# Kernel optimization log

Hardware: AMD Instinct MI355X
Metric: run time of the kernel (lower is better)

## Reference

```python
import jax, jax.numpy as jnp
import numpy as np

N = 50000          # nodes (ogbn-products-like subgraph)
E = 800000         # directed edges (avg degree 16)
F_IN, HID, HEADS, OUT = 100, 32, 4, 47
W1 = HID * HEADS   # 128
NEG_SLOPE = 0.2
BN_EPS = 1e-5


def _gatv2(x, src, dst, w_src, w_dst, att, bias, heads, ch):
    """GATv2Conv (PyG semantics, share_weights=False, concat).
    x: [N, F]; src/dst: [Etot] (self-loops already appended);
    w_src/w_dst: [F, heads*ch]; att: [heads, ch]; bias: [heads*ch].
    """
    n = x.shape[0]
    xl = (x @ w_src).reshape(n, heads, ch)   # source-side transform
    xr = (x @ w_dst).reshape(n, heads, ch)   # target-side transform
    # per-edge attention logits: a . leaky_relu(xl[j] + xr[i])  -> [E, heads]
    e = jnp.sum(jax.nn.leaky_relu(xl[src] + xr[dst], NEG_SLOPE) * att, axis=-1)
    # segment softmax over incoming edges of each destination node
    m = jax.ops.segment_max(e, dst, num_segments=n)          # [N, heads]
    ex = jnp.exp(e - m[dst])
    denom = jax.ops.segment_sum(ex, dst, num_segments=n)     # [N, heads]
    alpha = ex / denom[dst]                                  # [E, heads]
    # weighted scatter-add aggregation of source features
    out = jax.ops.segment_sum(alpha[:, :, None] * xl[src], dst, num_segments=n)
    return out.reshape(n, heads * ch) + bias


def _bn_eval(x, g, b, m, v):
    return (x - m) * jax.lax.rsqrt(v + BN_EPS) * g + b


def setup_inputs() -> dict:
    key = jax.random.key(0)
    ks = jax.random.split(key, 32)
    s = 0.1
    inp = {
        "x": jax.random.normal(ks[0], (N, F_IN), jnp.float32),
        "edge_index": jax.random.randint(ks[1], (2, E), 0, N, dtype=jnp.int32),
        "w1_src": jax.random.normal(ks[2], (F_IN, W1), jnp.float32) * s,
        "w1_dst": jax.random.normal(ks[3], (F_IN, W1), jnp.float32) * s,
        "att1": jax.random.normal(ks[4], (HEADS, HID), jnp.float32) * s,
        "b1": jnp.zeros((W1,), jnp.float32),
        "bn1_g": jnp.ones((W1,), jnp.float32),
        "bn1_b": jnp.zeros((W1,), jnp.float32),
        "bn1_m": jax.random.normal(ks[5], (W1,), jnp.float32) * 0.05,
        "bn1_v": jax.random.uniform(ks[6], (W1,), jnp.float32, 0.5, 1.5),
        "res0_w": jax.random.normal(ks[7], (F_IN, W1), jnp.float32) * s,
        "res0_b": jnp.zeros((W1,), jnp.float32),
        "w2_src": jax.random.normal(ks[8], (W1, W1), jnp.float32) * s,
        "w2_dst": jax.random.normal(ks[9], (W1, W1), jnp.float32) * s,
        "att2": jax.random.normal(ks[10], (HEADS, HID), jnp.float32) * s,
        "b2": jnp.zeros((W1,), jnp.float32),
        "bn2_g": jnp.ones((W1,), jnp.float32),
        "bn2_b": jnp.zeros((W1,), jnp.float32),
        "bn2_m": jax.random.normal(ks[11], (W1,), jnp.float32) * 0.05,
        "bn2_v": jax.random.uniform(ks[12], (W1,), jnp.float32, 0.5, 1.5),
        # layer 3: 128 -> 47, heads=1
        "w3_src": jax.random.normal(ks[13], (W1, OUT), jnp.float32) * s,
        "w3_dst": jax.random.normal(ks[14], (W1, OUT), jnp.float32) * s,
        "att3": jax.random.normal(ks[15], (1, OUT), jnp.float32) * s,
        "b3": jnp.zeros((OUT,), jnp.float32),
        "bn3_g": jnp.ones((OUT,), jnp.float32),
        "bn3_b": jnp.zeros((OUT,), jnp.float32),
        "bn3_m": jax.random.normal(ks[16], (OUT,), jnp.float32) * 0.05,
        "bn3_v": jax.random.uniform(ks[17], (OUT,), jnp.float32, 0.5, 1.5),
        "res2_w": jax.random.normal(ks[18], (W1, OUT), jnp.float32) * s,
        "res2_b": jnp.zeros((OUT,), jnp.float32),
    }
    return inp


def reference(x, edge_index,
              w1_src, w1_dst, att1, b1, bn1_g, bn1_b, bn1_m, bn1_v, res0_w, res0_b,
              w2_src, w2_dst, att2, b2, bn2_g, bn2_b, bn2_m, bn2_v,
              w3_src, w3_dst, att3, b3, bn3_g, bn3_b, bn3_m, bn3_v, res2_w, res2_b):
    # add self-loops (PyG GATv2Conv default add_self_loops=True)
    loops = jnp.arange(x.shape[0], dtype=edge_index.dtype)
    src = jnp.concatenate([edge_index[0], loops])
    dst = jnp.concatenate([edge_index[1], loops])

    # layer 1 + linear residual + BN + relu (eval mode: no dropout)
    h = _gatv2(x, src, dst, w1_src, w1_dst, att1, b1, HEADS, HID)
    h = h + (x @ res0_w + res0_b)
    h = jax.nn.relu(_bn_eval(h, bn1_g, bn1_b, bn1_m, bn1_v))

    # layer 2 + identity residual + BN + relu
    h2 = _gatv2(h, src, dst, w2_src, w2_dst, att2, b2, HEADS, HID)
    h2 = h2 + h
    h2 = jax.nn.relu(_bn_eval(h2, bn2_g, bn2_b, bn2_m, bn2_v))

    # layer 3 (heads=1) + linear residual + BN (no relu/dropout on last layer)
    out = _gatv2(h2, src, dst, w3_src, w3_dst, att3, b3, 1, OUT)
    out = out + (h2 @ res2_w + res2_b)
    out = _bn_eval(out, bn3_g, bn3_b, bn3_m, bn3_v)
    return out
```

## Files before the change

kernel.cpp:

```cpp
#include <hip/hip_runtime.h>
#include <math.h>

#define BN_EPS 1e-5f
#define SLOT 96
#define LN16 2.7725887f

typedef _Float16 h2 __attribute__((ext_vector_type(2)));
typedef _Float16 h8 __attribute__((ext_vector_type(8)));
typedef float f2v __attribute__((ext_vector_type(2)));
typedef float float4v __attribute__((ext_vector_type(4)));

static __device__ inline h2 bit_h2(unsigned u) {
    union { unsigned u; h2 h; } c; c.u = u; return c.h;
}
static __device__ inline unsigned bit_u(h2 h) {
    union { unsigned u; h2 h; } c; c.h = h; return c.u;
}

template <int CTRL>
static __device__ inline float dpp_add(float x) {
    int y = __builtin_amdgcn_update_dpp(0, __float_as_int(x), CTRL, 0xF, 0xF, true);
    return x + __int_as_float(y);
}
static __device__ inline float red8_dpp(float t) {
    t = dpp_add<0xB1>(t); t = dpp_add<0x4E>(t); t = dpp_add<0x141>(t);
    return t;
}
static __device__ inline float red16_dpp(float t) {
    t = dpp_add<0xB1>(t); t = dpp_add<0x4E>(t); t = dpp_add<0x141>(t);
    t = dpp_add<0x140>(t);
    return t;
}

static __device__ inline void pack_one(int idx,
                                       const float* p0, const float* p1,
                                       const float* p2,
                                       int w0, int w1, int w2,
                                       int Ksrc, int Ncat,
                                       _Float16* out) {
    int k = idx / Ncat, n = idx - k * Ncat;
    float v = 0.f;
    if (k < Ksrc) {
        if (n < w0) v = p0[(size_t)k * w0 + n];
        else if (n < w0 + w1) v = p1[(size_t)k * w1 + (n - w0)];
        else if (w2 > 0 && n < w0 + w1 + w2) v = p2[(size_t)k * w2 + (n - w0 - w1)];
    }
    int kt = k >> 5, kr = k & 31;
    int quad = kr >> 3, j = kr & 7;
    int nt = n >> 4, nr = n & 15;
    int ntiles = Ncat >> 4;
    out[((size_t)(kt * ntiles + nt) * 64 + quad * 16 + nr) * 8 + j] = (_Float16)v;
}

__global__ __launch_bounds__(256) void prep_scat_k(
    const int* __restrict__ src, const int* __restrict__ dst, int E, int Etot,
    int* __restrict__ cnt, int* __restrict__ esrc, int scatBlocks,
    const float* __restrict__ x, _Float16* __restrict__ A, int N,
    const float* __restrict__ w1s, const float* __restrict__ w1d,
    const float* __restrict__ r0w, const float* __restrict__ w2s,
    const float* __restrict__ w2d, const float* __restrict__ w3s,
    const float* __restrict__ w3d, const float* __restrict__ r2w,
    _Float16* __restrict__ Wb1, _Float16* __restrict__ Wb2,
    _Float16* __restrict__ Wb3) {
    if ((int)blockIdx.x < scatBlocks) {
        int i = blockIdx.x * 256 + threadIdx.x;
        if (i < Etot) {
            int d = (i < E) ? dst[i] : (i - E);
            int s = (i < E) ? src[i] : (i - E);
            int pos = atomicAdd(&cnt[d], 1);
            esrc[(size_t)d * SLOT + pos] = s << 9;
        }
        return;
    }
    const int S1 = 128 * 384, S2 = 128 * 256, S3 = 128 * 144;
    int convTot = N * 128;
    int idx = (blockIdx.x - scatBlocks) * 256 + threadIdx.x;
    if (idx < convTot) {
        int n = idx >> 7, k = idx & 127;
        A[idx] = (_Float16)(k < 100 ? x[(size_t)n * 100 + k] : 0.f);
        return;
    }
    int p = idx - convTot;
    if (p < S1) pack_one(p, w1s, w1d, r0w, 128, 128, 128, 100, 384, Wb1);
    else if (p < S1 + S2) pack_one(p - S1, w2s, w2d, nullptr, 128, 128, 0, 128, 256, Wb2);
    else if (p < S1 + S2 + S3) pack_one(p - S1 - S2, w3s, w3d, r2w, 47, 47, 47, 128, 144, Wb3);
}

template <int NT>
__global__ __launch_bounds__(256) void mfma_gemm(const _Float16* __restrict__ A,
                                                 const _Float16* __restrict__ Bp,
                                                 _Float16* __restrict__ XLR,
                                                 float* __restrict__ RES,
                                                 int M, int Kpad, int Ncat,
                                                 int ncat_valid, int res_off,
                                                 int bf_remap, int bf_shift,
                                                 int bf_stride, int res_stride) {
    int wid = (blockIdx.x * 256 + threadIdx.x) >> 6;
    int lane = threadIdx.x & 63;
    int ngroups = Ncat / (16 * NT);
    int mtiles = M >> 4;
    int mt = wid / ngroups;
    int ng = wid - mt * ngroups;
    if (mt >= mtiles) return;
    int quad = lane >> 4;
    int nr = lane & 15;
    int row = mt * 16 + nr;
    int ntiles = Ncat >> 4;

    float4v acc[NT];
#pragma unroll
    for (int t = 0; t < NT; t++) acc[t] = (float4v){0.f, 0.f, 0.f, 0.f};

    for (int k0 = 0; k0 < Kpad; k0 += 32) {
        h8 a = *(const h8*)(A + (size_t)row * Kpad + k0 + quad * 8);
        int kt = k0 >> 5;
        const _Float16* bbase =
            Bp + ((size_t)(kt * ntiles + ng * NT) * 64 + lane) * 8;
#pragma unroll
        for (int t = 0; t < NT; t++) {
            h8 b = *(const h8*)(bbase + (size_t)t * 64 * 8);
            acc[t] = __builtin_amdgcn_mfma_f32_16x16x32_f16(a, b, acc[t], 0, 0, 0);
        }
    }
    int rowb = mt * 16 + quad * 4;
#pragma unroll
    for (int t = 0; t < NT; t++) {
        int col = (ng * NT + t) * 16 + nr;
        if (col >= ncat_valid) continue;
        if (col < res_off) {
            int bc = (col >= bf_remap) ? col + bf_shift : col;
#pragma unroll
            for (int r = 0; r < 4; r++)
                XLR[(size_t)(rowb + r) * bf_stride + bc] = (_Float16)acc[t][r];
        } else {
            int rc = col - res_off;
#pragma unroll
            for (int r = 0; r < 4; r++)
                RES[(size_t)(rowb + r) * res_stride + rc] = acc[t][r];
        }
    }
}

__global__ __launch_bounds__(256) void gat_agg4_fused(
    const int* __restrict__ cnt, const int* __restrict__ esrc,
    const _Float16* __restrict__ xlr, const float* __restrict__ att,
    const float* __restrict__ RES, const float* __restrict__ resB,
    const float* __restrict__ bias,
    const float* __restrict__ g, const float* __restrict__ bb,
    const float* __restrict__ mm, const float* __restrict__ vv,
    _Float16* __restrict__ hbf, int N, int mode) {
    int d = blockIdx.x * 4 + (threadIdx.x >> 6);
    if (d >= N) return;
    int lane = threadIdx.x & 63;
    int half = lane >> 5;
    int gl = lane & 31;
    int c0 = gl * 4;
    const char* xb = (const char*)xlr + c0 * 2;
    const h2 NS = {(_Float16)0.2f, (_Float16)0.2f};

    uint2 xrv = *(const uint2*)(xb + (size_t)d * 512 + 256);
    h2 xr01 = bit_h2(xrv.x), xr23 = bit_h2(xrv.y);
    float4 af = *(const float4*)(att + c0);
    h2 at01 = {(_Float16)af.x, (_Float16)af.y};
    h2 at23 = {(_Float16)af.z, (_Float16)af.w};

    int beg = d * SLOT;
    int end = beg + cnt[d];
    float den = 0.f;
    h2 acc01 = {(_Float16)0.f, (_Float16)0.f};
    h2 acc23 = acc01;
    int j = beg;
    for (; j + 4 <= end; j += 4) {
        int o0 = esrc[j + half];
        int o1 = esrc[j + 2 + half];
        uint2 u0 = *(const uint2*)(xb + o0);
        uint2 u1 = *(const uint2*)(xb + o1);
        h2 a01 = bit_h2(u0.x), a23 = bit_h2(u0.y);
        h2 b01 = bit_h2(u1.x), b23 = bit_h2(u1.y);
        h2 v01 = a01 + xr01, v23 = a23 + xr23;
        h2 w01 = b01 + xr01, w23 = b23 + xr23;
        v01 = __builtin_elementwise_max(v01, v01 * NS);
        v23 = __builtin_elementwise_max(v23, v23 * NS);
        w01 = __builtin_elementwise_max(w01, w01 * NS);
        w23 = __builtin_elementwise_max(w23, w23 * NS);
        h2 t2a = v01 * at01 + v23 * at23;
        h2 t2b = w01 * at01 + w23 * at23;
        f2v ta = __builtin_convertvector(t2a, f2v);
        f2v tb = __builtin_convertvector(t2b, f2v);
        float t0 = ta.x + ta.y;
        float t1 = tb.x + tb.y;
        t0 = red8_dpp(t0);
        t1 = red8_dpp(t1);
        float p0 = __expf(t0 - LN16);
        float p1 = __expf(t1 - LN16);
        den += p0 + p1;
        h2 P0 = {(_Float16)p0, (_Float16)p0};
        h2 P1 = {(_Float16)p1, (_Float16)p1};
        acc01 = P0 * a01 + acc01;
        acc23 = P0 * a23 + acc23;
        acc01 = P1 * b01 + acc01;
        acc23 = P1 * b23 + acc23;
    }
    for (; j < end; j += 2) {
        int jj = j + half;
        bool act = jj < end;
        int o = esrc[act ? jj : (end - 1)];
        uint2 u0 = *(const uint2*)(xb + o);
        h2 a01 = bit_h2(u0.x), a23 = bit_h2(u0.y);
        h2 v01 = a01 + xr01, v23 = a23 + xr23;
        v01 = __builtin_elementwise_max(v01, v01 * NS);
        v23 = __builtin_elementwise_max(v23, v23 * NS);
        h2 t2 = v01 * at01 + v23 * at23;
        f2v tf = __builtin_convertvector(t2, f2v);
        float t = tf.x + tf.y;
        t = red8_dpp(t);
        float p = act ? __expf(t - LN16) : 0.f;
        den += p;
        h2 P = {(_Float16)p, (_Float16)p};
        acc01 = P * a01 + acc01;
        acc23 = P * a23 + acc23;
    }
    den += __shfl_xor(den, 32);
    f2v c01 = __builtin_convertvector(acc01, f2v);
    f2v c23 = __builtin_convertvector(acc23, f2v);
    float f0 = c01.x, f1 = c01.y, fA = c23.x, fB = c23.y;
    f0 += __shfl_xor(f0, 32);
    f1 += __shfl_xor(f1, 32);
    fA += __shfl_xor(fA, 32);
    fB += __shfl_xor(fB, 32);

    if (half == 0) {
        float inv = 1.f / den;
        float4 bi = *(const float4*)(bias + c0);
        float o0 = f0 * inv + bi.x;
        float o1 = f1 * inv + bi.y;
        float o2 = fA * inv + bi.z;
        float o3 = fB * inv + bi.w;
        if (mode == 1) {
            float4 r = *(const float4*)(RES + (size_t)d * 128 + c0);
            float4 rb = *(const float4*)(resB + c0);
            o0 += r.x + rb.x; o1 += r.y + rb.y;
            o2 += r.z + rb.z; o3 += r.w + rb.w;
        } else {
            uint2 hv = *(const uint2*)(hbf + (size_t)d * 128 + c0);
            f2v g01 = __builtin_convertvector(bit_h2(hv.x), f2v);
            f2v g23 = __builtin_convertvector(bit_h2(hv.y), f2v);
            o0 += g01.x; o1 += g01.y; o2 += g23.x; o3 += g23.y;
        }
        float4 gm = *(const float4*)(mm + c0);
        float4 gv = *(const float4*)(vv + c0);
        float4 gg = *(const float4*)(g + c0);
        float4 gb = *(const float4*)(bb + c0);
        o0 = fmaxf((o0 - gm.x) * rsqrtf(gv.x + BN_EPS) * gg.x + gb.x, 0.f);
        o1 = fmaxf((o1 - gm.y) * rsqrtf(gv.y + BN_EPS) * gg.y + gb.y, 0.f);
        o2 = fmaxf((o2 - gm.z) * rsqrtf(gv.z + BN_EPS) * gg.z + gb.z, 0.f);
        o3 = fmaxf((o3 - gm.w) * rsqrtf(gv.w + BN_EPS) * gg.w + gb.w, 0.f);
        h2 s01 = {(_Float16)o0, (_Float16)o1};
        h2 s23 = {(_Float16)o2, (_Float16)o3};
        uint2 w;
        w.x = bit_u(s01);
        w.y = bit_u(s23);
        *(uint2*)(hbf + (size_t)d * 128 + c0) = w;
    }
}

__global__ __launch_bounds__(256) void gat_agg1_fused(
    const int* __restrict__ cnt, const int* __restrict__ esrc,
    const _Float16* __restrict__ xlr, const float* __restrict__ att,
    const float* __restrict__ RES, const float* __restrict__ resB,
    const float* __restrict__ bias,
    const float* __restrict__ g, const float* __restrict__ bb,
    const float* __restrict__ mm, const float* __restrict__ vv,
    float* __restrict__ out, int N) {
    int d = blockIdx.x * 4 + (threadIdx.x >> 6);
    if (d >= N) return;
    int lane = threadIdx.x & 63;
    int gl = lane & 15, grp = lane >> 4;
    const char* xb = (const char*)xlr + gl * 8;
    const h2 NS = {(_Float16)0.2f, (_Float16)0.2f};

    uint2 xrv = *(const uint2*)(xb + (size_t)d * 256 + 128);
    h2 xr01 = bit_h2(xrv.x), xr23 = bit_h2(xrv.y);
    float atf[4];
#pragma unroll
    for (int k = 0; k < 4; k++) {
        int c = gl * 4 + k;
        atf[k] = (c < 47) ? att[c] : 0.f;
    }
    h2 at01 = {(_Float16)atf[0], (_Float16)atf[1]};
    h2 at23 = {(_Float16)atf[2], (_Float16)atf[3]};

    int beg = d * SLOT;
    int end = beg + cnt[d];
    float den = 0.f;
    h2 acc01 = {(_Float16)0.f, (_Float16)0.f};
    h2 acc23 = acc01;
    int j = beg + grp;
    for (; j + 4 < end; j += 8) {
        int o0 = esrc[j] >> 1;
        int o1 = esrc[j + 4] >> 1;
        uint2 u0 = *(const uint2*)(xb + o0);
        uint2 u1 = *(const uint2*)(xb + o1);
        h2 a01 = bit_h2(u0.x), a23 = bit_h2(u0.y);
        h2 b01 = bit_h2(u1.x), b23 = bit_h2(u1.y);
        h2 v01 = a01 + xr01, v23 = a23 + xr23;
        h2 w01 = b01 + xr01, w23 = b23 + xr23;
        v01 = __builtin_elementwise_max(v01, v01 * NS);
        v23 = __builtin_elementwise_max(v23, v23 * NS);
        w01 = __builtin_elementwise_max(w01, w01 * NS);
        w23 = __builtin_elementwise_max(w23, w23 * NS);
        h2 t2a = v01 * at01 + v23 * at23;
        h2 t2b = w01 * at01 + w23 * at23;
        f2v ta = __builtin_convertvector(t2a, f2v);
        f2v tb = __builtin_convertvector(t2b, f2v);
        float t0 = ta.x + ta.y;
        float t1 = tb.x + tb.y;
        t0 = red16_dpp(t0);
        t1 = red16_dpp(t1);
        float p0 = __expf(t0 - LN16);
        float p1 = __expf(t1 - LN16);
        den += p0 + p1;
        h2 P0 = {(_Float16)p0, (_Float16)p0};
        h2 P1 = {(_Float16)p1, (_Float16)p1};
        acc01 = P0 * a01 + acc01;
        acc23 = P0 * a23 + acc23;
        acc01 = P1 * b01 + acc01;
        acc23 = P1 * b23 + acc23;
    }
    if (j < end) {
        int o = esrc[j] >> 1;
        uint2 u0 = *(const uint2*)(xb + o);
        h2 a01 = bit_h2(u0.x), a23 = bit_h2(u0.y);
        h2 v01 = a01 + xr01, v23 = a23 + xr23;
        v01 = __builtin_elementwise_max(v01, v01 * NS);
        v23 = __builtin_elementwise_max(v23, v23 * NS);
        h2 t2 = v01 * at01 + v23 * at23;
        f2v tf = __builtin_convertvector(t2, f2v);
        float t = tf.x + tf.y;
        t = red16_dpp(t);
        float p = __expf(t - LN16);
        den += p;
        h2 P = {(_Float16)p, (_Float16)p};
        acc01 = P * a01 + acc01;
        acc23 = P * a23 + acc23;
    }
    den += __shfl_xor(den, 16);
    den += __shfl_xor(den, 32);
    f2v c01 = __builtin_convertvector(acc01, f2v);
    f2v c23 = __builtin_convertvector(acc23, f2v);
    float f[4] = {c01.x, c01.y, c23.x, c23.y};
#pragma unroll
    for (int k = 0; k < 4; k++) {
        f[k] += __shfl_xor(f[k], 16);
        f[k] += __shfl_xor(f[k], 32);
    }
    if (grp == 0 && gl < 12) {
        float inv = 1.f / den;
#pragma unroll
        for (int k = 0; k < 4; k++) {
            int c = gl * 4 + k;
            if (c < 47) {
                float o = f[k] * inv + bias[c] + RES[(size_t)d * 48 + c] + resB[c];
                o = (o - mm[c]) * rsqrtf(vv[c] + BN_EPS) * g[c] + bb[c];
                out[(size_t)d * 47 + c] = o;
            }
        }
    }
}

extern "C" void kernel_launch(void* const* d_in, const int* in_sizes, int n_in,
                              void* d_out, int out_size, void* d_ws, size_t ws_size,
                              hipStream_t stream) {
    const float* x      = (const float*)d_in[0];
    const int*   ei     = (const int*)d_in[1];
    const float* w1_src = (const float*)d_in[2];
    const float* w1_dst = (const float*)d_in[3];
    const float* att1   = (const float*)d_in[4];
    const float* b1     = (const float*)d_in[5];
    const float* bn1_g  = (const float*)d_in[6];
    const float* bn1_b  = (const float*)d_in[7];
    const float* bn1_m  = (const float*)d_in[8];
    const float* bn1_v  = (const float*)d_in[9];
    const float* res0_w = (const float*)d_in[10];
    const float* res0_b = (const float*)d_in[11];
    const float* w2_src = (const float*)d_in[12];
    const float* w2_dst = (const float*)d_in[13];
    const float* att2   = (const float*)d_in[14];
    const float* b2     = (const float*)d_in[15];
    const float* bn2_g  = (const float*)d_in[16];
    const float* bn2_b  = (const float*)d_in[17];
    const float* bn2_m  = (const float*)d_in[18];
    const float* bn2_v  = (const float*)d_in[19];
    const float* w3_src = (const float*)d_in[20];
    const float* w3_dst = (const float*)d_in[21];
    const float* att3   = (const float*)d_in[22];
    const float* b3     = (const float*)d_in[23];
    const float* bn3_g  = (const float*)d_in[24];
    const float* bn3_b  = (const float*)d_in[25];
    const float* bn3_m  = (const float*)d_in[26];
    const float* bn3_v  = (const float*)d_in[27];
    const float* res2_w = (const float*)d_in[28];
    const float* res2_b = (const float*)d_in[29];

    const int F_IN = 100;
    const int KP = 128;
    const int NC1 = 384, NC2 = 256, NC3 = 144;
    int N = in_sizes[0] / F_IN;
    int E = in_sizes[1] / 2;
    int Etot = E + N;
    const int* src = ei;
    const int* dst = ei + E;

    float* ws = (float*)d_ws;
    size_t o = 0;
    _Float16* XLR = (_Float16*)(ws + o); o += (size_t)N * 128;
    float* B_res = ws + o; o += (size_t)N * 128;
    _Float16* A_h = (_Float16*)(ws + o); o += (size_t)N * 64;
    _Float16* Wb1 = (_Float16*)(ws + o); o += (size_t)KP * NC1 / 2;
    _Float16* Wb2 = (_Float16*)(ws + o); o += (size_t)KP * NC2 / 2;
    _Float16* Wb3 = (_Float16*)(ws + o); o += (size_t)KP * NC3 / 2;
    int* I_cnt  = (int*)(ws + o); o += N;
    int* I_esrc = (int*)(ws + o); o += (size_t)N * SLOT + 4;
    (void)ws_size; (void)n_in; (void)out_size;

    int mtiles = (N + 15) / 16;
    int aggGrid = (N + 3) / 4;

    hipMemsetAsync(I_cnt, 0, (size_t)N * sizeof(int), stream);

    {
        int sb = (Etot + 255) / 256;
        int prepTot = N * KP + KP * (NC1 + NC2 + NC3);
        int pb = (prepTot + 255) / 256;
        prep_scat_k<<<sb + pb, 256, 0, stream>>>(
            src, dst, E, Etot, I_cnt, I_esrc, sb, x, A_h, N,
            w1_src, w1_dst, res0_w, w2_src, w2_dst, w3_src, w3_dst, res2_w,
            Wb1, Wb2, Wb3);
    }

    {
        int waves = mtiles * (NC1 / 64);
        mfma_gemm<4><<<(waves + 3) / 4, 256, 0, stream>>>(
            A_h, Wb1, XLR, B_res, N, KP, NC1, 384, 256, 384, 0, 256, 128);
    }
    gat_agg4_fused<<<aggGrid, 256, 0, stream>>>(
        I_cnt, I_esrc, XLR, att1, B_res, res0_b, b1,
        bn1_g, bn1_b, bn1_m, bn1_v, A_h, N, 1);

    {
        int waves = mtiles * (NC2 / 64);
        mfma_gemm<4><<<(waves + 3) / 4, 256, 0, stream>>>(
            A_h, Wb2, XLR, B_res, N, KP, NC2, 256, 256, 256, 0, 256, 128);
    }
    gat_agg4_fused<<<aggGrid, 256, 0, stream>>>(
        I_cnt, I_esrc, XLR, att2, nullptr, nullptr, b2,
        bn2_g, bn2_b, bn2_m, bn2_v, A_h, N, 2);

    {
        int waves = mtiles * (NC3 / 48);
        mfma_gemm<3><<<(waves + 3) / 4, 256, 0, stream>>>(
            A_h, Wb3, XLR, B_res, N, KP, NC3, 141, 94, 47, 17, 128, 48);
    }
    gat_agg1_fused<<<aggGrid, 256, 0, stream>>>(
        I_cnt, I_esrc, XLR, att3, B_res, res2_b, b3,
        bn3_g, bn3_b, bn3_m, bn3_v, (float*)d_out, N);
}
```

Measured before the change: 394.4 us.

## Have each GEMM wave cover all column groups, and unroll aggregation gathers by eight

The MFMA GEMM now assigns one wave per 16-row tile. Each wave loads its A fragments once into registers (K fixed at 128) and loops over every column group, so A is not reloaded per column group. The trade-off is a much smaller grid with more serial work per wave. The 4-head aggregation loop now issues four gathers before computing on them, to give more memory-level parallelism. The esrc scatter writes use nontemporal stores.

```diff
diff --git a/kernel.cpp b/kernel.cpp
--- a/kernel.cpp
+++ b/kernel.cpp
@@ -68,7 +68,7 @@
             int d = (i < E) ? dst[i] : (i - E);
             int s = (i < E) ? src[i] : (i - E);
             int pos = atomicAdd(&cnt[d], 1);
-            esrc[(size_t)d * SLOT + pos] = s << 9;
+            __builtin_nontemporal_store(s << 9, &esrc[(size_t)d * SLOT + pos]);
         }
         return;
     }
@@ -91,52 +91,55 @@
                                                  const _Float16* __restrict__ Bp,
                                                  _Float16* __restrict__ XLR,
                                                  float* __restrict__ RES,
-                                                 int M, int Kpad, int Ncat,
+                                                 int M, int Ncat,
                                                  int ncat_valid, int res_off,
                                                  int bf_remap, int bf_shift,
                                                  int bf_stride, int res_stride) {
-    int wid = (blockIdx.x * 256 + threadIdx.x) >> 6;
+    int mt = (blockIdx.x * 256 + threadIdx.x) >> 6;
     int lane = threadIdx.x & 63;
+    int mtiles = M >> 4;
+    if (mt >= mtiles) return;
     int ngroups = Ncat / (16 * NT);
-    int mtiles = M >> 4;
-    int mt = wid / ngroups;
-    int ng = wid - mt * ngroups;
-    if (mt >= mtiles) return;
+    int ntiles = Ncat >> 4;
     int quad = lane >> 4;
     int nr = lane & 15;
     int row = mt * 16 + nr;
-    int ntiles = Ncat >> 4;
-
-    float4v acc[NT];
-#pragma unroll
-    for (int t = 0; t < NT; t++) acc[t] = (float4v){0.f, 0.f, 0.f, 0.f};
-
-    for (int k0 = 0; k0 < Kpad; k0 += 32) {
-        h8 a = *(const h8*)(A + (size_t)row * Kpad + k0 + quad * 8);
-        int kt = k0 >> 5;
-        const _Float16* bbase =
-            Bp + ((size_t)(kt * ntiles + ng * NT) * 64 + lane) * 8;
+
+    h8 a[4];
+#pragma unroll
+    for (int kt = 0; kt < 4; kt++)
+        a[kt] = *(const h8*)(A + (size_t)row * 128 + kt * 32 + quad * 8);
+
+    int rowb = mt * 16 + quad * 4;
+    for (int ng = 0; ng < ngroups; ng++) {
+        float4v acc[NT];
+#pragma unroll
+        for (int t = 0; t < NT; t++) acc[t] = (float4v){0.f, 0.f, 0.f, 0.f};
+#pragma unroll
+        for (int kt = 0; kt < 4; kt++) {
+            const _Float16* bbase =
+                Bp + ((size_t)(kt * ntiles + ng * NT) * 64 + lane) * 8;
+#pragma unroll
+            for (int t = 0; t < NT; t++) {
+                h8 b = *(const h8*)(bbase + (size_t)t * 512);
+                acc[t] = __builtin_amdgcn_mfma_f32_16x16x32_f16(a[kt], b, acc[t], 0, 0, 0);
+            }
+        }
 #pragma unroll
         for (int t = 0; t < NT; t++) {
-            h8 b = *(const h8*)(bbase + (size_t)t * 64 * 8);
-            acc[t] = __builtin_amdgcn_mfma_f32_16x16x32_f16(a, b, acc[t], 0, 0, 0);
-        }
-    }
-    int rowb = mt * 16 + quad * 4;
-#pragma unroll
-    for (int t = 0; t < NT; t++) {
-        int col = (ng * NT + t) * 16 + nr;
-        if (col >= ncat_valid) continue;
-        if (col < res_off) {
-            int bc = (col >= bf_remap) ? col + bf_shift : col;
-#pragma unroll
-            for (int r = 0; r < 4; r++)
-                XLR[(size_t)(rowb + r) * bf_stride + bc] = (_Float16)acc[t][r];
-        } else {
-            int rc = col - res_off;
-#pragma unroll
-            for (int r = 0; r < 4; r++)
-                RES[(size_t)(rowb + r) * res_stride + rc] = acc[t][r];
+            int col = (ng * NT + t) * 16 + nr;
+            if (col >= ncat_valid) continue;
+            if (col < res_off) {
+                int bc = (col >= bf_remap) ? col + bf_shift : col;
+#pragma unroll
+                for (int r = 0; r < 4; r++)
+                    XLR[(size_t)(rowb + r) * bf_stride + bc] = (_Float16)acc[t][r];
+            } else {
+                int rc = col - res_off;
+#pragma unroll
+                for (int r = 0; r < 4; r++)
+                    RES[(size_t)(rowb + r) * res_stride + rc] = acc[t][r];
+            }
         }
     }
 }
@@ -170,36 +173,28 @@
     h2 acc01 = {(_Float16)0.f, (_Float16)0.f};
     h2 acc23 = acc01;
     int j = beg;
-    for (; j + 4 <= end; j += 4) {
-        int o0 = esrc[j + half];
-        int o1 = esrc[j + 2 + half];
-        uint2 u0 = *(const uint2*)(xb + o0);
-        uint2 u1 = *(const uint2*)(xb + o1);
-        h2 a01 = bit_h2(u0.x), a23 = bit_h2(u0.y);
-        h2 b01 = bit_h2(u1.x), b23 = bit_h2(u1.y);
-        h2 v01 = a01 + xr01, v23 = a23 + xr23;
-        h2 w01 = b01 + xr01, w23 = b23 + xr23;
-        v01 = __builtin_elementwise_max(v01, v01 * NS);
-        v23 = __builtin_elementwise_max(v23, v23 * NS);
-        w01 = __builtin_elementwise_max(w01, w01 * NS);
-        w23 = __builtin_elementwise_max(w23, w23 * NS);
-        h2 t2a = v01 * at01 + v23 * at23;
-        h2 t2b = w01 * at01 + w23 * at23;
-        f2v ta = __builtin_convertvector(t2a, f2v);
-        f2v tb = __builtin_convertvector(t2b, f2v);
-        float t0 = ta.x + ta.y;
-        float t1 = tb.x + tb.y;
-        t0 = red8_dpp(t0);
-        t1 = red8_dpp(t1);
-        float p0 = __expf(t0 - LN16);
-        float p1 = __expf(t1 - LN16);
-        den += p0 + p1;
-        h2 P0 = {(_Float16)p0, (_Float16)p0};
-        h2 P1 = {(_Float16)p1, (_Float16)p1};
-        acc01 = P0 * a01 + acc01;
-        acc23 = P0 * a23 + acc23;
-        acc01 = P1 * b01 + acc01;
-        acc23 = P1 * b23 + acc23;
+    for (; j + 8 <= end; j += 8) {
+        uint2 u[4];
+#pragma unroll
+        for (int q = 0; q < 4; q++) {
+            int o = esrc[j + 2 * q + half];
+            u[q] = *(const uint2*)(xb + o);
+        }
+#pragma unroll
+        for (int q = 0; q < 4; q++) {
+            h2 a01 = bit_h2(u[q].x), a23 = bit_h2(u[q].y);
+            h2 v01 = a01 + xr01, v23 = a23 + xr23;
+            v01 = __builtin_elementwise_max(v01, v01 * NS);
+            v23 = __builtin_elementwise_max(v23, v23 * NS);
+            h2 t2 = v01 * at01 + v23 * at23;
+            f2v tf = __builtin_convertvector(t2, f2v);
+            float t = red8_dpp(tf.x + tf.y);
+            float p = __expf(t - LN16);
+            den += p;
+            h2 P = {(_Float16)p, (_Float16)p};
+            acc01 = P * a01 + acc01;
+            acc23 = P * a23 + acc23;
+        }
     }
     for (; j < end; j += 2) {
         int jj = j + half;
@@ -212,8 +207,7 @@
         v23 = __builtin_elementwise_max(v23, v23 * NS);
         h2 t2 = v01 * at01 + v23 * at23;
         f2v tf = __builtin_convertvector(t2, f2v);
-        float t = tf.x + tf.y;
-        t = red8_dpp(t);
+        float t = red8_dpp(tf.x + tf.y);
         float p = act ? __expf(t - LN16) : 0.f;
         den += p;
         h2 P = {(_Float16)p, (_Float16)p};
@@ -313,10 +307,8 @@
         h2 t2b = w01 * at01 + w23 * at23;
         f2v ta = __builtin_convertvector(t2a, f2v);
         f2v tb = __builtin_convertvector(t2b, f2v);
-        float t0 = ta.x + ta.y;
-        float t1 = tb.x + tb.y;
-        t0 = red16_dpp(t0);
-        t1 = red16_dpp(t1);
+        float t0 = red16_dpp(ta.x + ta.y);
+        float t1 = red16_dpp(tb.x + tb.y);
         float p0 = __expf(t0 - LN16);
         float p1 = __expf(t1 - LN16);
         den += p0 + p1;
@@ -336,8 +328,7 @@
         v23 = __builtin_elementwise_max(v23, v23 * NS);
         h2 t2 = v01 * at01 + v23 * at23;
         f2v tf = __builtin_convertvector(t2, f2v);
-        float t = tf.x + tf.y;
-        t = red16_dpp(t);
+        float t = red16_dpp(tf.x + tf.y);
         float p = __expf(t - LN16);
         den += p;
         h2 P = {(_Float16)p, (_Float16)p};
@@ -425,6 +416,7 @@
 
     int mtiles = (N + 15) / 16;
     int aggGrid = (N + 3) / 4;
+    int gemmGrid = (mtiles + 3) / 4;
 
     hipMemsetAsync(I_cnt, 0, (size_t)N * sizeof(int), stream);
 
@@ -438,29 +430,20 @@
             Wb1, Wb2, Wb3);
     }
 
-    {
-        int waves = mtiles * (NC1 / 64);
-        mfma_gemm<4><<<(waves + 3) / 4, 256, 0, stream>>>(
-            A_h, Wb1, XLR, B_res, N, KP, NC1, 384, 256, 384, 0, 256, 128);
-    }
+    mfma_gemm<4><<<gemmGrid, 256, 0, stream>>>(
+        A_h, Wb1, XLR, B_res, N, NC1, 384, 256, 384, 0, 256, 128);
     gat_agg4_fused<<<aggGrid, 256, 0, stream>>>(
         I_cnt, I_esrc, XLR, att1, B_res, res0_b, b1,
         bn1_g, bn1_b, bn1_m, bn1_v, A_h, N, 1);
 
-    {
-        int waves = mtiles * (NC2 / 64);
-        mfma_gemm<4><<<(waves + 3) / 4, 256, 0, stream>>>(
-            A_h, Wb2, XLR, B_res, N, KP, NC2, 256, 256, 256, 0, 256, 128);
-    }
+    mfma_gemm<4><<<gemmGrid, 256, 0, stream>>>(
+        A_h, Wb2, XLR, B_res, N, NC2, 256, 256, 256, 0, 256, 128);
     gat_agg4_fused<<<aggGrid, 256, 0, stream>>>(
         I_cnt, I_esrc, XLR, att2, nullptr, nullptr, b2,
         bn2_g, bn2_b, bn2_m, bn2_v, A_h, N, 2);
 
-    {
-        int waves = mtiles * (NC3 / 48);
-        mfma_gemm<3><<<(waves + 3) / 4, 256, 0, stream>>>(
-            A_h, Wb3, XLR, B_res, N, KP, NC3, 141, 94, 47, 17, 128, 48);
-    }
+    mfma_gemm<3><<<gemmGrid, 256, 0, stream>>>(
+        A_h, Wb3, XLR, B_res, N, NC3, 141, 94, 47, 17, 128, 48);
     gat_agg1_fused<<<aggGrid, 256, 0, stream>>>(
         I_cnt, I_esrc, XLR, att3, B_res, res2_b, b3,
         bn3_g, bn3_b, bn3_m, bn3_v, (float*)d_out, N);
```

Result: no change. 389.9 us (-1.1%).
